# Optimization experiments

Hardware: AMD Instinct MI355X
Metric: run time of the kernel (lower is better)

## Reference

```python
import jax, jax.numpy as jnp
import numpy as np

D_MODEL = 512
NHEAD = 8
DK = D_MODEL // NHEAD
DIM_FF = 2048
LN_EPS = 1e-5


def setup_inputs() -> dict:
    key = jax.random.key(0)
    ks = jax.random.split(key, 12)
    B, L = 8, 1024
    s = 1.0 / np.sqrt(D_MODEL)
    sf = 1.0 / np.sqrt(DIM_FF)
    return {
        "x": jax.random.normal(ks[0], (B, L, D_MODEL), jnp.float32),
        "key_padding_mask": jnp.zeros((B, L), dtype=bool),
        "bias": jax.random.normal(ks[1], (B, L, L), jnp.float32),
        # projection weights stored [in, out] so y = x @ W + b (matches torch Linear math)
        "Wq": jax.random.normal(ks[2], (D_MODEL, D_MODEL), jnp.float32) * s,
        "bq": jnp.zeros((D_MODEL,), jnp.float32),
        "Wk": jax.random.normal(ks[3], (D_MODEL, D_MODEL), jnp.float32) * s,
        "bk": jnp.zeros((D_MODEL,), jnp.float32),
        "Wv": jax.random.normal(ks[4], (D_MODEL, D_MODEL), jnp.float32) * s,
        "bv": jnp.zeros((D_MODEL,), jnp.float32),
        "Wo": jax.random.normal(ks[5], (D_MODEL, D_MODEL), jnp.float32) * s,
        "bo": jnp.zeros((D_MODEL,), jnp.float32),
        "ln1_g": jnp.ones((D_MODEL,), jnp.float32),
        "ln1_b": jnp.zeros((D_MODEL,), jnp.float32),
        "W1": jax.random.normal(ks[6], (D_MODEL, DIM_FF), jnp.float32) * s,
        "b1": jnp.zeros((DIM_FF,), jnp.float32),
        "W2": jax.random.normal(ks[7], (DIM_FF, D_MODEL), jnp.float32) * sf,
        "b2": jnp.zeros((D_MODEL,), jnp.float32),
        "ln2_g": jnp.ones((D_MODEL,), jnp.float32),
        "ln2_b": jnp.zeros((D_MODEL,), jnp.float32),
    }


def _layernorm(x, g, b):
    mu = jnp.mean(x, axis=-1, keepdims=True)
    var = jnp.mean(jnp.square(x - mu), axis=-1, keepdims=True)
    return (x - mu) * jax.lax.rsqrt(var + LN_EPS) * g + b


def reference(x, key_padding_mask, bias, Wq, bq, Wk, bk, Wv, bv, Wo, bo,
              ln1_g, ln1_b, W1, b1, W2, b2, ln2_g, ln2_b):
    B, L, H = x.shape
    residual = x
    # [B, L, D] -> [B, nhead, L, dk]
    q = (x @ Wq + bq).reshape(B, L, NHEAD, DK).transpose(0, 2, 1, 3)
    k = (x @ Wk + bk).reshape(B, L, NHEAD, DK).transpose(0, 2, 1, 3)
    v = (x @ Wv + bv).reshape(B, L, NHEAD, DK).transpose(0, 2, 1, 3)
    scores = jnp.einsum("bhqd,bhkd->bhqk", q, k) / np.sqrt(DK)
    scores = scores + bias[:, None, :, :]
    scores = jnp.where(key_padding_mask[:, None, None, :], -jnp.inf, scores)
    attn = jax.nn.softmax(scores, axis=-1)  # dropout p=0 (eval)
    out = jnp.einsum("bhqk,bhkd->bhqd", attn, v)
    out = out.transpose(0, 2, 1, 3).reshape(B, L, H)
    out = out @ Wo + bo
    x = _layernorm(residual + out, ln1_g, ln1_b)
    residual = x
    h = jax.nn.relu(x @ W1 + b1)
    x = h @ W2 + b2
    return _layernorm(residual + x, ln2_g, ln2_b)
```

## Files before the change

### kernel.cpp

```cpp
#include <hip/hip_runtime.h>
#include <math.h>

#define NHEAD 8
#define DKD 64
#define DMODEL 512
#define LSEQ 1024
#define NBL 8192

typedef __attribute__((ext_vector_type(8))) short bf8;
typedef __attribute__((ext_vector_type(4))) float f4;

__device__ inline unsigned short f2bf(float f) {
    union { float f; unsigned u; } v; v.f = f;
    unsigned r = v.u + 0x7FFFu + ((v.u >> 16) & 1u);
    return (unsigned short)(r >> 16);
}

__device__ __forceinline__ unsigned cvtpk(float lo, float hi) {
    unsigned r;
    asm("v_cvt_pk_bf16_f32 %0, %1, %2" : "=v"(r) : "v"(lo), "v"(hi));
    return r;
}

__device__ __forceinline__ void gload16(const void* g, void* l) {
    __builtin_amdgcn_global_load_lds(
        (const __attribute__((address_space(1))) unsigned int*)g,
        (__attribute__((address_space(3))) unsigned int*)l, 16, 0, 0);
}

__global__ __launch_bounds__(256) void conv_bf16(
    const float* __restrict__ in, unsigned short* __restrict__ out, int n)
{
    int i = (blockIdx.x * 256 + threadIdx.x) * 4;
    if (i >= n) return;
    float4 v = *(const float4*)(in + i);
    ushort4 o;
    o.x = f2bf(v.x); o.y = f2bf(v.y); o.z = f2bf(v.z); o.w = f2bf(v.w);
    *(ushort4*)(out + i) = o;
}

__device__ __forceinline__ void do_transpose(
    const float* __restrict__ W, unsigned short* __restrict__ Wt,
    int K, int N, int bx, int by)
{
    __shared__ float tile[64][65];
    const int k0 = by * 64, n0 = bx * 64;
    const int c = threadIdx.x & 63, r0 = (threadIdx.x >> 6) * 16;
    #pragma unroll
    for (int i = 0; i < 16; ++i)
        tile[r0 + i][c] = W[(size_t)(k0 + r0 + i) * N + n0 + c];
    __syncthreads();
    #pragma unroll
    for (int i = 0; i < 16; ++i)
        Wt[(size_t)(n0 + r0 + i) * K + k0 + c] = f2bf(tile[c][r0 + i]);
}

__global__ __launch_bounds__(256) void prep_weights(
    const float* __restrict__ Wq, const float* __restrict__ Wk,
    const float* __restrict__ Wv, const float* __restrict__ Wo,
    const float* __restrict__ W1, const float* __restrict__ W2,
    const float* __restrict__ bq, const float* __restrict__ bk,
    const float* __restrict__ bv,
    unsigned short* __restrict__ Wqkv, unsigned short* __restrict__ Wot,
    unsigned short* __restrict__ W1t, unsigned short* __restrict__ W2t,
    float* __restrict__ bqkv)
{
    int j = blockIdx.x;
    if (j < 256) {
        int which = j >> 6, tt = j & 63;
        const float* src = which == 0 ? Wq : which == 1 ? Wk : which == 2 ? Wv : Wo;
        unsigned short* dst = which == 0 ? Wqkv : which == 1 ? (Wqkv + 262144)
                            : which == 2 ? (Wqkv + 524288) : Wot;
        do_transpose(src, dst, 512, 512, tt & 7, tt >> 3);
    } else if (j < 512) {
        int tt = j - 256;
        do_transpose(W1, W1t, 512, 2048, tt & 31, tt >> 5);
    } else if (j < 768) {
        int tt = j - 512;
        do_transpose(W2, W2t, 2048, 512, tt & 7, tt >> 3);
    } else {
        for (int c = threadIdx.x; c < 1536; c += 256)
            bqkv[c] = c < 512 ? bq[c] : c < 1024 ? bk[c - 512] : bv[c - 1024];
    }
}

template<int BN>
__global__ __launch_bounds__(256) void mfma_gemm(
    const unsigned short* __restrict__ A, const unsigned short* __restrict__ Bt,
    const float* __restrict__ bias, const float* __restrict__ resid,
    void* __restrict__ outp, int M, int N, int K, int relu, int outmode,
    unsigned short* __restrict__ qs, unsigned short* __restrict__ ks,
    unsigned short* __restrict__ vts)
{
    __shared__ uint4 As[2][1024];
    __shared__ uint4 Bs[2][BN * 8];
    constexpr int NB = BN / 32;

    const int t = threadIdx.x;
    const int lane = t & 63, w = t >> 6;
    const int g = lane >> 4, r15 = lane & 15;
    const int wr = w >> 1, wc = w & 1;
    const int rowBase = blockIdx.y * 128, colBase = blockIdx.x * BN;

    f4 acc[4][NB] = {};

    const int r   = t >> 3;
    const int chs = (t & 7) ^ (r & 7);
    const unsigned short* Ag0 = A  + (size_t)(rowBase + r) * K + chs * 8;
    const unsigned short* Bg0 = Bt + (size_t)(colBase + r) * K + chs * 8;

    auto stage = [&](int buf, int k0) {
        unsigned short* Al = (unsigned short*)As[buf] + (w * 8) * 64;
        unsigned short* Bl = (unsigned short*)Bs[buf] + (w * 8) * 64;
        const unsigned short* Ag = Ag0 + k0;
        const unsigned short* Bg = Bg0 + k0;
        #pragma unroll
        for (int p = 0; p < 4; ++p)
            gload16(Ag + (size_t)(p * 32) * K, Al + p * 32 * 64);
        #pragma unroll
        for (int p = 0; p < NB; ++p)
            gload16(Bg + (size_t)(p * 32) * K, Bl + p * 32 * 64);
    };

    const int nst = K >> 6;
    stage(0, 0);
    __syncthreads();

    for (int it = 0; it < nst; ++it) {
        const int cur = it & 1;
        if (it + 1 < nst) stage(cur ^ 1, (it + 1) << 6);
        #pragma unroll
        for (int kk = 0; kk < 2; ++kk) {
            bf8 af[4], bfr[NB];
            #pragma unroll
            for (int m = 0; m < 4; ++m) {
                int ra = wr * 64 + m * 16 + r15;
                af[m] = *(const bf8*)&As[cur][ra * 8 + ((kk * 4 + g) ^ (ra & 7))];
            }
            #pragma unroll
            for (int n = 0; n < NB; ++n) {
                int rb = wc * (BN / 2) + n * 16 + r15;
                bfr[n] = *(const bf8*)&Bs[cur][rb * 8 + ((kk * 4 + g) ^ (rb & 7))];
            }
            #pragma unroll
            for (int m = 0; m < 4; ++m)
                #pragma unroll
                for (int n = 0; n < NB; ++n)
                    acc[m][n] = __builtin_amdgcn_mfma_f32_16x16x32_bf16(
                        af[m], bfr[n], acc[m][n], 0, 0, 0);
        }
        __syncthreads();
    }

    #pragma unroll
    for (int m = 0; m < 4; ++m) {
        #pragma unroll
        for (int n = 0; n < NB; ++n) {
            int col = colBase + wc * (BN / 2) + n * 16 + r15;
            float bv = bias[col];
            #pragma unroll
            for (int rr = 0; rr < 4; ++rr) {
                int row = rowBase + wr * 64 + m * 16 + g * 4 + rr;
                float v = acc[m][n][rr] + bv;
                if (relu) v = fmaxf(v, 0.f);
                if (outmode == 0) {
                    size_t idx = (size_t)row * N + col;
                    if (resid) v += resid[idx];
                    ((float*)outp)[idx] = v;
                } else if (outmode == 1) {
                    ((unsigned short*)outp)[(size_t)row * N + col] = f2bf(v);
                } else {
                    int sel = col >> 9, hd = col & 511;
                    int h = hd >> 6, dk = hd & 63;
                    int b = row >> 10, l = row & 1023;
                    unsigned short bw = f2bf(v);
                    size_t bh = (size_t)(b * NHEAD + h);
                    if (sel == 0)      qs[(bh * LSEQ + l) * DKD + dk] = bw;
                    else if (sel == 1) ks[(bh * LSEQ + l) * DKD + dk] = bw;
                    else               vts[(bh * DKD + dk) * LSEQ + l] = bw;
                }
            }
        }
    }
}

struct TileRegs { float4 b[2][4]; unsigned mk[4]; };

__device__ __forceinline__ void load_tile_regs(
    TileRegs& tr, const float* bR0, const float* bR1,
    const unsigned char* mrow, int key0, int g)
{
    #pragma unroll
    for (int m = 0; m < 4; ++m) {
        tr.b[0][m] = *(const float4*)(bR0 + key0 + m * 16 + g * 4);
        tr.b[1][m] = *(const float4*)(bR1 + key0 + m * 16 + g * 4);
        tr.mk[m]   = *(const unsigned*)(mrow + key0 + m * 16 + g * 4);
    }
}

__device__ __forceinline__ void attn_tile(
    const uint4* __restrict__ Kb, const uint4* __restrict__ Vb,
    const TileRegs& tr, bf8 (&qf)[2][2], f4 (&oacc)[2][4],
    float (&mrun)[2], float (&lsum)[2],
    unsigned short* Pw, int g, int r15)
{
    f4 sacc[2][4] = {};
    __builtin_amdgcn_s_setprio(1);
    #pragma unroll
    for (int kk = 0; kk < 2; ++kk)
        #pragma unroll
        for (int m = 0; m < 4; ++m) {
            int row = m * 16 + r15;
            bf8 kf = *(const bf8*)&Kb[row * 8 + ((kk * 4 + g) ^ (row & 7))];
            sacc[0][m] = __builtin_amdgcn_mfma_f32_16x16x32_bf16(kf, qf[0][kk], sacc[0][m], 0, 0, 0);
            sacc[1][m] = __builtin_amdgcn_mfma_f32_16x16x32_bf16(kf, qf[1][kk], sacc[1][m], 0, 0, 0);
        }
    __builtin_amdgcn_s_setprio(0);

    float madd[16];
    #pragma unroll
    for (int m = 0; m < 4; ++m) {
        unsigned mku = tr.mk[m];
        #pragma unroll
        for (int j = 0; j < 4; ++j)
            madd[m * 4 + j] = ((mku >> (8 * j)) & 0xffu) ? -1e30f : 0.f;
    }

    #pragma unroll
    for (int u = 0; u < 2; ++u) {
        float s[16];
        float pmax = -1e30f;
        #pragma unroll
        for (int m = 0; m < 4; ++m) {
            const float* bvp = (const float*)&tr.b[u][m];
            #pragma unroll
            for (int j = 0; j < 4; ++j) {
                float sv = fmaf(sacc[u][m][j], 0.125f, bvp[j] + madd[m * 4 + j]);
                s[m * 4 + j] = sv;
                pmax = fmaxf(pmax, sv);
            }
        }
        pmax = fmaxf(pmax, __shfl_xor(pmax, 16));
        pmax = fmaxf(pmax, __shfl_xor(pmax, 32));

        if (!__all(pmax <= mrun[u] + 8.f)) {
            float mnew = fmaxf(mrun[u], pmax);
            float scale = __expf(mrun[u] - mnew);
            lsum[u] *= scale;
            #pragma unroll
            for (int m = 0; m < 4; ++m)
                #pragma unroll
                for (int j = 0; j < 4; ++j) oacc[u][m][j] *= scale;
            mrun[u] = mnew;
        }

        float psum = 0.f;
        #pragma unroll
        for (int i = 0; i < 16; ++i) { s[i] = __expf(s[i] - mrun[u]); psum += s[i]; }
        psum += __shfl_xor(psum, 16);
        psum += __shfl_xor(psum, 32);
        lsum[u] += psum;

        #pragma unroll
        for (int m = 0; m < 4; ++m) {
            uint2 pk;
            pk.x = cvtpk(s[m * 4 + 0], s[m * 4 + 1]);
            pk.y = cvtpk(s[m * 4 + 2], s[m * 4 + 3]);
            int off = ((u * 16 + r15) * 128 + m * 32 + g * 8) ^ ((r15 & 7) << 4);
            *(uint2*)((char*)Pw + off) = pk;
        }
    }

    #pragma unroll
    for (int kk = 0; kk < 2; ++kk) {
        bf8 pf[2];
        #pragma unroll
        for (int u = 0; u < 2; ++u) {
            int off = ((u * 16 + r15) * 128 + kk * 64 + g * 16) ^ ((r15 & 7) << 4);
            pf[u] = *(const bf8*)((char*)Pw + off);
        }
        __builtin_amdgcn_s_setprio(1);
        #pragma unroll
        for (int m = 0; m < 4; ++m) {
            int row = m * 16 + r15;
            bf8 vf = *(const bf8*)&Vb[row * 8 + ((kk * 4 + g) ^ (row & 7))];
            oacc[0][m] = __builtin_amdgcn_mfma_f32_16x16x32_bf16(vf, pf[0], oacc[0][m], 0, 0, 0);
            oacc[1][m] = __builtin_amdgcn_mfma_f32_16x16x32_bf16(vf, pf[1], oacc[1][m], 0, 0, 0);
        }
        __builtin_amdgcn_s_setprio(0);
    }
}

__global__ __launch_bounds__(256) void attn_mfma(
    const unsigned short* __restrict__ Qg, const unsigned short* __restrict__ Kg,
    const unsigned short* __restrict__ Vtg, const float* __restrict__ bias,
    const unsigned char* __restrict__ mask, unsigned short* __restrict__ Ob)
{
    __shared__ uint4 Ks[2][512];
    __shared__ uint4 Vs[2][512];
    __shared__ unsigned int Pb[4096];

    const int t = threadIdx.x;
    const int lane = t & 63, w = t >> 6;
    const int g = lane >> 4, r15 = lane & 15;

    const int p = blockIdx.x;
    const int logical = (p & 7) * 64 + (p >> 3);
    const int bh = logical >> 3, qt = logical & 7;
    const int b = bh >> 3, h = bh & 7;
    const int qbase = qt * 128 + w * 32;

    bf8 qf[2][2];
    #pragma unroll
    for (int u = 0; u < 2; ++u) {
        const unsigned short* qp = Qg + ((size_t)bh * LSEQ + qbase + u * 16 + r15) * DKD + g * 8;
        qf[u][0] = *(const bf8*)qp;
        qf[u][1] = *(const bf8*)(qp + 32);
    }

    float mrun[2] = {-1e30f, -1e30f}, lsum[2] = {0.f, 0.f};
    f4 oacc[2][4] = {};

    const int sr  = t >> 3;
    const int chs = (t & 7) ^ (sr & 7);
    unsigned short* Pw = (unsigned short*)(Pb + w * 1024);

    const size_t kBase = (size_t)bh * LSEQ * DKD;
    const size_t vBase = (size_t)bh * DKD * LSEQ;

    const float* bR0 = bias + ((size_t)b << 20) + (size_t)(qbase + r15) * LSEQ;
    const float* bR1 = bias + ((size_t)b << 20) + (size_t)(qbase + 16 + r15) * LSEQ;
    const unsigned char* mrow = mask + b * LSEQ;

    auto stage = [&](uint4* Kbuf, uint4* Vbuf, int key0) {
        const unsigned short* Kgp = Kg  + kBase + (size_t)(key0 + sr) * DKD + chs * 8;
        const unsigned short* Vgp = Vtg + vBase + (size_t)sr * LSEQ + key0 + chs * 8;
        unsigned short* Kl = (unsigned short*)Kbuf + (w * 8) * 64;
        unsigned short* Vl = (unsigned short*)Vbuf + (w * 8) * 64;
        gload16(Kgp, Kl);
        gload16(Kgp + (size_t)32 * DKD, Kl + 32 * 64);
        gload16(Vgp, Vl);
        gload16(Vgp + (size_t)32 * LSEQ, Vl + 32 * 64);
    };

    TileRegs trA, trB;
    load_tile_regs(trA, bR0, bR1, mrow, 0, g);
    stage(Ks[0], Vs[0], 0);
    __syncthreads();

    for (int kt2 = 0; kt2 < 8; ++kt2) {
        const int keyE = kt2 * 128;
        stage(Ks[1], Vs[1], keyE + 64);
        load_tile_regs(trB, bR0, bR1, mrow, keyE + 64, g);
        attn_tile(Ks[0], Vs[0], trA, qf, oacc, mrun, lsum, Pw, g, r15);
        __syncthreads();
        if (kt2 < 7) {
            stage(Ks[0], Vs[0], keyE + 128);
            load_tile_regs(trA, bR0, bR1, mrow, keyE + 128, g);
        }
        attn_tile(Ks[1], Vs[1], trB, qf, oacc, mrun, lsum, Pw, g, r15);
        __syncthreads();
    }

    #pragma unroll
    for (int u = 0; u < 2; ++u) {
        float inv = 1.f / lsum[u];
        unsigned short* op = Ob + ((size_t)b * LSEQ + qbase + u * 16 + r15) * DMODEL + h * DKD;
        #pragma unroll
        for (int m = 0; m < 4; ++m) {
            ushort4 o4;
            o4.x = f2bf(oacc[u][m][0] * inv);
            o4.y = f2bf(oacc[u][m][1] * inv);
            o4.z = f2bf(oacc[u][m][2] * inv);
            o4.w = f2bf(oacc[u][m][3] * inv);
            *(ushort4*)(op + m * 16 + g * 4) = o4;
        }
    }
}

__global__ __launch_bounds__(256) void ln_kernel(
    const float* __restrict__ in, const float* __restrict__ g,
    const float* __restrict__ bt, float* __restrict__ out,
    unsigned short* __restrict__ outb)
{
    const int row  = blockIdx.x * 4 + (threadIdx.x >> 6);
    const int lane = threadIdx.x & 63;
    const float* rp = in + (size_t)row * DMODEL + lane * 8;
    float4 x0 = *(const float4*)rp;
    float4 x1 = *(const float4*)(rp + 4);
    float xs[8] = {x0.x, x0.y, x0.z, x0.w, x1.x, x1.y, x1.z, x1.w};

    float sum = 0.f;
    #pragma unroll
    for (int i = 0; i < 8; ++i) sum += xs[i];
    #pragma unroll
    for (int off = 32; off; off >>= 1) sum += __shfl_xor(sum, off);
    float mu = sum * (1.f / 512.f);

    float vs = 0.f;
    #pragma unroll
    for (int i = 0; i < 8; ++i) { float d = xs[i] - mu; vs += d * d; }
    #pragma unroll
    for (int off = 32; off; off >>= 1) vs += __shfl_xor(vs, off);
    float rs = rsqrtf(vs * (1.f / 512.f) + 1e-5f);

    const float* gp = g  + lane * 8;
    const float* bp = bt + lane * 8;
    float4 g0 = *(const float4*)gp, g1 = *(const float4*)(gp + 4);
    float4 b0 = *(const float4*)bp, b1 = *(const float4*)(bp + 4);
    float gs[8] = {g0.x, g0.y, g0.z, g0.w, g1.x, g1.y, g1.z, g1.w};
    float bs[8] = {b0.x, b0.y, b0.z, b0.w, b1.x, b1.y, b1.z, b1.w};

    float res[8];
    #pragma unroll
    for (int i = 0; i < 8; ++i) res[i] = (xs[i] - mu) * rs * gs[i] + bs[i];

    float* op = out + (size_t)row * DMODEL + lane * 8;
    float4 r0 = {res[0], res[1], res[2], res[3]};
    float4 r1 = {res[4], res[5], res[6], res[7]};
    *(float4*)op       = r0;
    *(float4*)(op + 4) = r1;

    if (outb) {
        unsigned short* ob = outb + (size_t)row * DMODEL + lane * 8;
        ushort4 u0, u1;
        u0.x = f2bf(res[0]); u0.y = f2bf(res[1]); u0.z = f2bf(res[2]); u0.w = f2bf(res[3]);
        u1.x = f2bf(res[4]); u1.y = f2bf(res[5]); u1.z = f2bf(res[6]); u1.w = f2bf(res[7]);
        *(ushort4*)ob       = u0;
        *(ushort4*)(ob + 4) = u1;
    }
}

extern "C" void kernel_launch(void* const* d_in, const int* in_sizes, int n_in,
                              void* d_out, int out_size, void* d_ws, size_t ws_size,
                              hipStream_t stream)
{
    const float*         x    = (const float*)d_in[0];
    const unsigned char* mask = (const unsigned char*)d_in[1];
    const float*         bias = (const float*)d_in[2];
    const float* Wq = (const float*)d_in[3];
    const float* bq = (const float*)d_in[4];
    const float* Wk = (const float*)d_in[5];
    const float* bk = (const float*)d_in[6];
    const float* Wv = (const float*)d_in[7];
    const float* bv = (const float*)d_in[8];
    const float* Wo = (const float*)d_in[9];
    const float* bo = (const float*)d_in[10];
    const float* ln1g = (const float*)d_in[11];
    const float* ln1b = (const float*)d_in[12];
    const float* W1 = (const float*)d_in[13];
    const float* b1 = (const float*)d_in[14];
    const float* W2 = (const float*)d_in[15];
    const float* b2 = (const float*)d_in[16];
    const float* ln2g = (const float*)d_in[17];
    const float* ln2b = (const float*)d_in[18];

    char* W = (char*)d_ws;
    unsigned short* Qb   = (unsigned short*)(W);
    unsigned short* Kb   = (unsigned short*)(W + (8u << 20));
    unsigned short* Vtb  = (unsigned short*)(W + (16u << 20));
    unsigned short* Oball= (unsigned short*)(W + (24u << 20));
    unsigned short* hb   = (unsigned short*)(W);
    float*          y12  = (float*)(W + (32u << 20));
    float*          x1   = (float*)(W + (48u << 20));
    unsigned short* xb   = (unsigned short*)(W + (66u << 20));
    unsigned short* x1b  = xb;
    unsigned short* Wqkv = (unsigned short*)(W + (74u << 20));
    unsigned short* Wot  = (unsigned short*)(W + (76u << 20));
    unsigned short* W1t  = (unsigned short*)(W + (77u << 20));
    unsigned short* W2t  = (unsigned short*)(W + (79u << 20));
    float*          bqkv = (float*)(W + (81u << 20));
    float*          outp = (float*)d_out;

    conv_bf16<<<dim3(4096), dim3(256), 0, stream>>>(x, xb, NBL * DMODEL);
    prep_weights<<<dim3(769), dim3(256), 0, stream>>>(
        Wq, Wk, Wv, Wo, W1, W2, bq, bk, bv, Wqkv, Wot, W1t, W2t, bqkv);

    mfma_gemm<128><<<dim3(12, 64), dim3(256), 0, stream>>>(
        xb, Wqkv, bqkv, nullptr, nullptr, NBL, 1536, 512, 0, 2, Qb, Kb, Vtb);

    attn_mfma<<<dim3(512), dim3(256), 0, stream>>>(Qb, Kb, Vtb, bias, mask, Oball);

    mfma_gemm<64><<<dim3(8, 64), dim3(256), 0, stream>>>(
        Oball, Wot, bo, x, y12, NBL, 512, 512, 0, 0, nullptr, nullptr, nullptr);

    ln_kernel<<<dim3(NBL / 4), dim3(256), 0, stream>>>(y12, ln1g, ln1b, x1, x1b);

    mfma_gemm<128><<<dim3(16, 64), dim3(256), 0, stream>>>(
        x1b, W1t, b1, nullptr, hb, NBL, 2048, 512, 1, 1, nullptr, nullptr, nullptr);

    mfma_gemm<64><<<dim3(8, 64), dim3(256), 0, stream>>>(
        hb, W2t, b2, x1, y12, NBL, 512, 2048, 0, 0, nullptr, nullptr, nullptr);

    ln_kernel<<<dim3(NBL / 4), dim3(256), 0, stream>>>(y12, ln2g, ln2b, outp, nullptr);
}
```

Baseline: 383.1 us.

## Precompute bf16 bias with folded mask and stage it through LDS in attention

A new pre-pass folds the key padding mask into the attention bias and writes it as bf16. The attention kernel then streams each bias tile into LDS with asynchronous global-to-LDS loads, double-buffered alongside K and V, instead of issuing per-thread fp32 register loads of bias and mask. Bias is reused across the 8 heads, so halving its width is meant to cut global and L2 traffic in the attention loop. The cost is an extra kernel pass over the full bias tensor, rounding the bias to bf16, and 32KB more LDS per block, which may reduce occupancy.

```diff
diff --git a/kernel.cpp b/kernel.cpp
--- a/kernel.cpp
+++ b/kernel.cpp
@@ -37,6 +37,32 @@
     ushort4 o;
     o.x = f2bf(v.x); o.y = f2bf(v.y); o.z = f2bf(v.z); o.w = f2bf(v.w);
     *(ushort4*)(out + i) = o;
+}
+
+__global__ __launch_bounds__(256) void biasmb_kernel(
+    const float* __restrict__ bias, const unsigned char* __restrict__ mask,
+    unsigned short* __restrict__ o)
+{
+    size_t flat = ((size_t)blockIdx.x * 256 + threadIdx.x) * 8;
+    int b = (int)(flat >> 20);
+    int k = (int)(flat & 1023);
+    float4 v0 = *(const float4*)(bias + flat);
+    float4 v1 = *(const float4*)(bias + flat + 4);
+    uint2 mk = *(const uint2*)(mask + b * 1024 + k);
+    float vs[8] = {v0.x, v0.y, v0.z, v0.w, v1.x, v1.y, v1.z, v1.w};
+    unsigned mw[2] = {mk.x, mk.y};
+    unsigned short os[8];
+    #pragma unroll
+    for (int j = 0; j < 8; ++j) {
+        unsigned mb = (mw[j >> 2] >> ((j & 3) * 8)) & 0xffu;
+        os[j] = f2bf(mb ? -1e30f : vs[j]);
+    }
+    uint4 pk;
+    pk.x = (unsigned)os[0] | ((unsigned)os[1] << 16);
+    pk.y = (unsigned)os[2] | ((unsigned)os[3] << 16);
+    pk.z = (unsigned)os[4] | ((unsigned)os[5] << 16);
+    pk.w = (unsigned)os[6] | ((unsigned)os[7] << 16);
+    *(uint4*)(o + flat) = pk;
 }
 
 __device__ __forceinline__ void do_transpose(
@@ -184,120 +210,14 @@
     }
 }
 
-struct TileRegs { float4 b[2][4]; unsigned mk[4]; };
-
-__device__ __forceinline__ void load_tile_regs(
-    TileRegs& tr, const float* bR0, const float* bR1,
-    const unsigned char* mrow, int key0, int g)
-{
-    #pragma unroll
-    for (int m = 0; m < 4; ++m) {
-        tr.b[0][m] = *(const float4*)(bR0 + key0 + m * 16 + g * 4);
-        tr.b[1][m] = *(const float4*)(bR1 + key0 + m * 16 + g * 4);
-        tr.mk[m]   = *(const unsigned*)(mrow + key0 + m * 16 + g * 4);
-    }
-}
-
-__device__ __forceinline__ void attn_tile(
-    const uint4* __restrict__ Kb, const uint4* __restrict__ Vb,
-    const TileRegs& tr, bf8 (&qf)[2][2], f4 (&oacc)[2][4],
-    float (&mrun)[2], float (&lsum)[2],
-    unsigned short* Pw, int g, int r15)
-{
-    f4 sacc[2][4] = {};
-    __builtin_amdgcn_s_setprio(1);
-    #pragma unroll
-    for (int kk = 0; kk < 2; ++kk)
-        #pragma unroll
-        for (int m = 0; m < 4; ++m) {
-            int row = m * 16 + r15;
-            bf8 kf = *(const bf8*)&Kb[row * 8 + ((kk * 4 + g) ^ (row & 7))];
-            sacc[0][m] = __builtin_amdgcn_mfma_f32_16x16x32_bf16(kf, qf[0][kk], sacc[0][m], 0, 0, 0);
-            sacc[1][m] = __builtin_amdgcn_mfma_f32_16x16x32_bf16(kf, qf[1][kk], sacc[1][m], 0, 0, 0);
-        }
-    __builtin_amdgcn_s_setprio(0);
-
-    float madd[16];
-    #pragma unroll
-    for (int m = 0; m < 4; ++m) {
-        unsigned mku = tr.mk[m];
-        #pragma unroll
-        for (int j = 0; j < 4; ++j)
-            madd[m * 4 + j] = ((mku >> (8 * j)) & 0xffu) ? -1e30f : 0.f;
-    }
-
-    #pragma unroll
-    for (int u = 0; u < 2; ++u) {
-        float s[16];
-        float pmax = -1e30f;
-        #pragma unroll
-        for (int m = 0; m < 4; ++m) {
-            const float* bvp = (const float*)&tr.b[u][m];
-            #pragma unroll
-            for (int j = 0; j < 4; ++j) {
-                float sv = fmaf(sacc[u][m][j], 0.125f, bvp[j] + madd[m * 4 + j]);
-                s[m * 4 + j] = sv;
-                pmax = fmaxf(pmax, sv);
-            }
-        }
-        pmax = fmaxf(pmax, __shfl_xor(pmax, 16));
-        pmax = fmaxf(pmax, __shfl_xor(pmax, 32));
-
-        if (!__all(pmax <= mrun[u] + 8.f)) {
-            float mnew = fmaxf(mrun[u], pmax);
-            float scale = __expf(mrun[u] - mnew);
-            lsum[u] *= scale;
-            #pragma unroll
-            for (int m = 0; m < 4; ++m)
-                #pragma unroll
-                for (int j = 0; j < 4; ++j) oacc[u][m][j] *= scale;
-            mrun[u] = mnew;
-        }
-
-        float psum = 0.f;
-        #pragma unroll
-        for (int i = 0; i < 16; ++i) { s[i] = __expf(s[i] - mrun[u]); psum += s[i]; }
-        psum += __shfl_xor(psum, 16);
-        psum += __shfl_xor(psum, 32);
-        lsum[u] += psum;
-
-        #pragma unroll
-        for (int m = 0; m < 4; ++m) {
-            uint2 pk;
-            pk.x = cvtpk(s[m * 4 + 0], s[m * 4 + 1]);
-            pk.y = cvtpk(s[m * 4 + 2], s[m * 4 + 3]);
-            int off = ((u * 16 + r15) * 128 + m * 32 + g * 8) ^ ((r15 & 7) << 4);
-            *(uint2*)((char*)Pw + off) = pk;
-        }
-    }
-
-    #pragma unroll
-    for (int kk = 0; kk < 2; ++kk) {
-        bf8 pf[2];
-        #pragma unroll
-        for (int u = 0; u < 2; ++u) {
-            int off = ((u * 16 + r15) * 128 + kk * 64 + g * 16) ^ ((r15 & 7) << 4);
-            pf[u] = *(const bf8*)((char*)Pw + off);
-        }
-        __builtin_amdgcn_s_setprio(1);
-        #pragma unroll
-        for (int m = 0; m < 4; ++m) {
-            int row = m * 16 + r15;
-            bf8 vf = *(const bf8*)&Vb[row * 8 + ((kk * 4 + g) ^ (row & 7))];
-            oacc[0][m] = __builtin_amdgcn_mfma_f32_16x16x32_bf16(vf, pf[0], oacc[0][m], 0, 0, 0);
-            oacc[1][m] = __builtin_amdgcn_mfma_f32_16x16x32_bf16(vf, pf[1], oacc[1][m], 0, 0, 0);
-        }
-        __builtin_amdgcn_s_setprio(0);
-    }
-}
-
 __global__ __launch_bounds__(256) void attn_mfma(
     const unsigned short* __restrict__ Qg, const unsigned short* __restrict__ Kg,
-    const unsigned short* __restrict__ Vtg, const float* __restrict__ bias,
-    const unsigned char* __restrict__ mask, unsigned short* __restrict__ Ob)
+    const unsigned short* __restrict__ Vtg, const unsigned short* __restrict__ biasMb,
+    unsigned short* __restrict__ Ob)
 {
     __shared__ uint4 Ks[2][512];
     __shared__ uint4 Vs[2][512];
+    __shared__ uint4 Bls[2][1024];
     __shared__ unsigned int Pb[4096];
 
     const int t = threadIdx.x;
@@ -321,44 +241,124 @@
     float mrun[2] = {-1e30f, -1e30f}, lsum[2] = {0.f, 0.f};
     f4 oacc[2][4] = {};
 
-    const int sr  = t >> 3;
-    const int chs = (t & 7) ^ (sr & 7);
+    const int sr   = t >> 3;
+    const int chs  = (t & 7) ^ (sr & 7);
+    const int brow = lane >> 3;
+    const int bch  = (lane & 7) ^ brow;
     unsigned short* Pw = (unsigned short*)(Pb + w * 1024);
 
     const size_t kBase = (size_t)bh * LSEQ * DKD;
     const size_t vBase = (size_t)bh * DKD * LSEQ;
-
-    const float* bR0 = bias + ((size_t)b << 20) + (size_t)(qbase + r15) * LSEQ;
-    const float* bR1 = bias + ((size_t)b << 20) + (size_t)(qbase + 16 + r15) * LSEQ;
-    const unsigned char* mrow = mask + b * LSEQ;
-
-    auto stage = [&](uint4* Kbuf, uint4* Vbuf, int key0) {
+    const unsigned short* bB = biasMb + ((size_t)b << 20);
+
+    auto stage = [&](int buf, int key0) {
         const unsigned short* Kgp = Kg  + kBase + (size_t)(key0 + sr) * DKD + chs * 8;
         const unsigned short* Vgp = Vtg + vBase + (size_t)sr * LSEQ + key0 + chs * 8;
-        unsigned short* Kl = (unsigned short*)Kbuf + (w * 8) * 64;
-        unsigned short* Vl = (unsigned short*)Vbuf + (w * 8) * 64;
+        unsigned short* Kl = (unsigned short*)Ks[buf] + (w * 8) * 64;
+        unsigned short* Vl = (unsigned short*)Vs[buf] + (w * 8) * 64;
         gload16(Kgp, Kl);
         gload16(Kgp + (size_t)32 * DKD, Kl + 32 * 64);
         gload16(Vgp, Vl);
         gload16(Vgp + (size_t)32 * LSEQ, Vl + 32 * 64);
+        unsigned short* Bl = (unsigned short*)Bls[buf] + w * 2048;
+        #pragma unroll
+        for (int pp = 0; pp < 4; ++pp) {
+            const unsigned short* Bgp = bB + (size_t)(qbase + pp * 8 + brow) * 1024
+                                      + key0 + bch * 8;
+            gload16(Bgp, Bl + pp * 512);
+        }
     };
 
-    TileRegs trA, trB;
-    load_tile_regs(trA, bR0, bR1, mrow, 0, g);
-    stage(Ks[0], Vs[0], 0);
+    stage(0, 0);
     __syncthreads();
 
-    for (int kt2 = 0; kt2 < 8; ++kt2) {
-        const int keyE = kt2 * 128;
-        stage(Ks[1], Vs[1], keyE + 64);
-        load_tile_regs(trB, bR0, bR1, mrow, keyE + 64, g);
-        attn_tile(Ks[0], Vs[0], trA, qf, oacc, mrun, lsum, Pw, g, r15);
-        __syncthreads();
-        if (kt2 < 7) {
-            stage(Ks[0], Vs[0], keyE + 128);
-            load_tile_regs(trA, bR0, bR1, mrow, keyE + 128, g);
-        }
-        attn_tile(Ks[1], Vs[1], trB, qf, oacc, mrun, lsum, Pw, g, r15);
+    for (int kt = 0; kt < 16; ++kt) {
+        const int cur = kt & 1;
+        if (kt < 15) stage(cur ^ 1, (kt + 1) * 64);
+
+        const char* Bw = (const char*)Bls[cur] + w * 4096;
+
+        f4 sacc[2][4] = {};
+        __builtin_amdgcn_s_setprio(1);
+        #pragma unroll
+        for (int kk = 0; kk < 2; ++kk)
+            #pragma unroll
+            for (int m = 0; m < 4; ++m) {
+                int row = m * 16 + r15;
+                bf8 kf = *(const bf8*)&Ks[cur][row * 8 + ((kk * 4 + g) ^ (row & 7))];
+                sacc[0][m] = __builtin_amdgcn_mfma_f32_16x16x32_bf16(kf, qf[0][kk], sacc[0][m], 0, 0, 0);
+                sacc[1][m] = __builtin_amdgcn_mfma_f32_16x16x32_bf16(kf, qf[1][kk], sacc[1][m], 0, 0, 0);
+            }
+        __builtin_amdgcn_s_setprio(0);
+
+        #pragma unroll
+        for (int u = 0; u < 2; ++u) {
+            float s[16];
+            float pmax = -1e30f;
+            #pragma unroll
+            for (int m = 0; m < 4; ++m) {
+                int off = (u * 16 + r15) * 128 + ((m * 32 + g * 8) ^ ((r15 & 7) << 4));
+                uint2 bv = *(const uint2*)(Bw + off);
+                float b0 = __uint_as_float(bv.x << 16);
+                float b1 = __uint_as_float(bv.x & 0xffff0000u);
+                float b2 = __uint_as_float(bv.y << 16);
+                float b3 = __uint_as_float(bv.y & 0xffff0000u);
+                s[m * 4 + 0] = fmaf(sacc[u][m][0], 0.125f, b0);
+                s[m * 4 + 1] = fmaf(sacc[u][m][1], 0.125f, b1);
+                s[m * 4 + 2] = fmaf(sacc[u][m][2], 0.125f, b2);
+                s[m * 4 + 3] = fmaf(sacc[u][m][3], 0.125f, b3);
+                #pragma unroll
+                for (int j = 0; j < 4; ++j) pmax = fmaxf(pmax, s[m * 4 + j]);
+            }
+            pmax = fmaxf(pmax, __shfl_xor(pmax, 16));
+            pmax = fmaxf(pmax, __shfl_xor(pmax, 32));
+
+            if (!__all(pmax <= mrun[u] + 8.f)) {
+                float mnew = fmaxf(mrun[u], pmax);
+                float scale = __expf(mrun[u] - mnew);
+                lsum[u] *= scale;
+                #pragma unroll
+                for (int m = 0; m < 4; ++m)
+                    #pragma unroll
+                    for (int j = 0; j < 4; ++j) oacc[u][m][j] *= scale;
+                mrun[u] = mnew;
+            }
+
+            float psum = 0.f;
+            #pragma unroll
+            for (int i = 0; i < 16; ++i) { s[i] = __expf(s[i] - mrun[u]); psum += s[i]; }
+            psum += __shfl_xor(psum, 16);
+            psum += __shfl_xor(psum, 32);
+            lsum[u] += psum;
+
+            #pragma unroll
+            for (int m = 0; m < 4; ++m) {
+                uint2 pk;
+                pk.x = cvtpk(s[m * 4 + 0], s[m * 4 + 1]);
+                pk.y = cvtpk(s[m * 4 + 2], s[m * 4 + 3]);
+                int off = ((u * 16 + r15) * 128 + m * 32 + g * 8) ^ ((r15 & 7) << 4);
+                *(uint2*)((char*)Pw + off) = pk;
+            }
+        }
+
+        #pragma unroll
+        for (int kk = 0; kk < 2; ++kk) {
+            bf8 pf[2];
+            #pragma unroll
+            for (int u = 0; u < 2; ++u) {
+                int off = ((u * 16 + r15) * 128 + kk * 64 + g * 16) ^ ((r15 & 7) << 4);
+                pf[u] = *(const bf8*)((char*)Pw + off);
+            }
+            __builtin_amdgcn_s_setprio(1);
+            #pragma unroll
+            for (int m = 0; m < 4; ++m) {
+                int row = m * 16 + r15;
+                bf8 vf = *(const bf8*)&Vs[cur][row * 8 + ((kk * 4 + g) ^ (row & 7))];
+                oacc[0][m] = __builtin_amdgcn_mfma_f32_16x16x32_bf16(vf, pf[0], oacc[0][m], 0, 0, 0);
+                oacc[1][m] = __builtin_amdgcn_mfma_f32_16x16x32_bf16(vf, pf[1], oacc[1][m], 0, 0, 0);
+            }
+            __builtin_amdgcn_s_setprio(0);
+        }
         __syncthreads();
     }
 
@@ -461,8 +461,9 @@
     unsigned short* Vtb  = (unsigned short*)(W + (16u << 20));
     unsigned short* Oball= (unsigned short*)(W + (24u << 20));
     unsigned short* hb   = (unsigned short*)(W);
+    unsigned short* biasMb=(unsigned short*)(W + (32u << 20));
     float*          y12  = (float*)(W + (32u << 20));
-    float*          x1   = (float*)(W + (48u << 20));
+    float*          x1   = (float*)(W + (49u << 20));
     unsigned short* xb   = (unsigned short*)(W + (66u << 20));
     unsigned short* x1b  = xb;
     unsigned short* Wqkv = (unsigned short*)(W + (74u << 20));
@@ -475,11 +476,12 @@
     conv_bf16<<<dim3(4096), dim3(256), 0, stream>>>(x, xb, NBL * DMODEL);
     prep_weights<<<dim3(769), dim3(256), 0, stream>>>(
         Wq, Wk, Wv, Wo, W1, W2, bq, bk, bv, Wqkv, Wot, W1t, W2t, bqkv);
+    biasmb_kernel<<<dim3(4096), dim3(256), 0, stream>>>(bias, mask, biasMb);
 
     mfma_gemm<128><<<dim3(12, 64), dim3(256), 0, stream>>>(
         xb, Wqkv, bqkv, nullptr, nullptr, NBL, 1536, 512, 0, 2, Qb, Kb, Vtb);
 
-    attn_mfma<<<dim3(512), dim3(256), 0, stream>>>(Qb, Kb, Vtb, bias, mask, Oball);
+    attn_mfma<<<dim3(512), dim3(256), 0, stream>>>(Qb, Kb, Vtb, biasMb, Oball);
 
     mfma_gemm<64><<<dim3(8, 64), dim3(256), 0, stream>>>(
         Oball, Wot, bo, x, y12, NBL, 512, 512, 0, 0, nullptr, nullptr, nullptr);
```

New measurement: 341.0 us. 11.0% less time.
